# Kernel optimization log

Hardware: AMD Instinct MI355X
Metric: run time of the kernel (lower is better)

Reference implementation:

```python
import jax, jax.numpy as jnp
import numpy as np

B, T, C = 4, 2048, 1024
WIN = 16


def setup_inputs() -> dict:
    key = jax.random.key(0)
    ks = jax.random.split(key, 5)
    s = 1.0 / np.sqrt(C)
    return {
        "x": jax.random.normal(ks[0], (B, T, C), dtype=jnp.float32),
        "Wq": jax.random.normal(ks[1], (C, C), dtype=jnp.float32) * s,
        "bq": jnp.zeros((C,), jnp.float32),
        "Wk": jax.random.normal(ks[2], (C, C), dtype=jnp.float32) * s,
        "bk": jnp.zeros((C,), jnp.float32),
        "Wv": jax.random.normal(ks[3], (C, C), dtype=jnp.float32) * s,
        "bv": jnp.zeros((C,), jnp.float32),
        "Wo": jax.random.normal(ks[4], (C, C), dtype=jnp.float32) * s,
        "bo": jnp.zeros((C,), jnp.float32),
        "window": WIN,
    }


def reference(x, Wq, bq, Wk, bk, Wv, bv, Wo, bo, window):
    Bn, Tn, Cn = x.shape
    half = window // 2
    W = 2 * half + 1  # keys per query (window [t-half, t+half])
    q = x @ Wq.T + bq
    k = x @ Wk.T + bk
    v = x @ Wv.T + bv
    offs = jnp.arange(-half, half + 1)              # [W]
    tpos = jnp.arange(Tn)                            # [T]
    idx = tpos[:, None] + offs[None, :]              # [T, W]
    valid = (idx >= 0) & (idx < Tn)                  # [T, W]
    idx_c = jnp.clip(idx, 0, Tn - 1)
    k_win = k[:, idx_c, :]                           # [B, T, W, C]
    v_win = v[:, idx_c, :]                           # [B, T, W, C]
    scale = 1.0 / jnp.sqrt(jnp.asarray(Cn, x.dtype))
    scores = jnp.einsum('btc,btwc->btw', q, k_win) * scale
    scores = jnp.where(valid[None, :, :], scores, jnp.finfo(x.dtype).min)
    attn = jax.nn.softmax(scores, axis=-1)           # [B, T, W]
    ctx = jnp.einsum('btw,btwc->btc', attn, v_win)   # [B, T, C]
    return ctx @ Wo.T + bo
```

## Files before the change

### kernel.cpp

```cpp
#include <hip/hip_runtime.h>
#include <cstdint>
#include <cstddef>

#define B_ 4
#define T_ 2048
#define C_ 1024
#define M_ (B_ * T_)
#define HALF_ 8
#define W_ 17
#define QKV_STRIDE 3072

typedef unsigned short u16;
typedef _Float16 half8 __attribute__((ext_vector_type(8)));
typedef _Float16 half2_t __attribute__((ext_vector_type(2)));
typedef float f32x16 __attribute__((ext_vector_type(16)));

__device__ __forceinline__ void gload_lds16(const u16* g, u16* l) {
#if __has_builtin(__builtin_amdgcn_global_load_lds)
    __builtin_amdgcn_global_load_lds(
        (const __attribute__((address_space(1))) void*)g,
        (__attribute__((address_space(3))) void*)l, 16, 0, 0);
#else
    *(uint4*)(l + (threadIdx.x & 63) * 8) = *(const uint4*)g;
#endif
}

__device__ __forceinline__ float dot16(half8 a, half8 b, float acc) {
#if __has_builtin(__builtin_amdgcn_fdot2)
    const half2_t* pa = (const half2_t*)&a;
    const half2_t* pb = (const half2_t*)&b;
#pragma unroll
    for (int e = 0; e < 4; ++e) acc = __builtin_amdgcn_fdot2(pa[e], pb[e], acc, false);
#else
#pragma unroll
    for (int e = 0; e < 8; ++e) acc += (float)a[e] * (float)b[e];
#endif
    return acc;
}

__global__ void prologue(const float* __restrict__ x,
                         const float* __restrict__ Wq, const float* __restrict__ Wk,
                         const float* __restrict__ Wv, const float* __restrict__ Wo,
                         const float* __restrict__ bq, const float* __restrict__ bk,
                         const float* __restrict__ bv,
                         u16* __restrict__ xh, u16* __restrict__ wcat,
                         u16* __restrict__ woh, float* __restrict__ bcat) {
    const int blk = blockIdx.x;
    if (blk >= 12288) {
        int i = (blk - 12288) * 256 + threadIdx.x;
        const float* src = (i < 1024) ? bq : (i < 2048) ? bk : bv;
        bcat[i] = src[i & 1023];
        return;
    }
    const float* src;
    u16* dst;
    int j;
    if (blk < 8192)       { src = x;  dst = xh;   j = blk * 256 + threadIdx.x; }
    else if (blk < 11264) {
        int bb = blk - 8192;
        int sel = bb >> 10;
        src = (sel == 0) ? Wq : (sel == 1) ? Wk : Wv;
        dst = wcat + ((size_t)sel << 20);
        j = (bb - (sel << 10)) * 256 + threadIdx.x;
    } else                { src = Wo; dst = woh;  j = (blk - 11264) * 256 + threadIdx.x; }
    float4 v = ((const float4*)src)[j];
    ushort4 o;
    _Float16 a = (_Float16)v.x; o.x = __builtin_bit_cast(unsigned short, a);
    _Float16 b = (_Float16)v.y; o.y = __builtin_bit_cast(unsigned short, b);
    _Float16 c = (_Float16)v.z; o.z = __builtin_bit_cast(unsigned short, c);
    _Float16 d = (_Float16)v.w; o.w = __builtin_bit_cast(unsigned short, d);
    ((ushort4*)dst)[j] = o;
}

__global__ __launch_bounds__(256) void gemm_nt_lds(
    const u16* __restrict__ A, const u16* __restrict__ Bw,
    const float* __restrict__ bias, u16* __restrict__ Cout,
    int Ndim, int Kdim)
{
    __shared__ __align__(16) u16 As[128 * 32];
    __shared__ __align__(16) u16 Bs[128 * 32];

    const int tid  = threadIdx.x;
    const int lane = tid & 63;
    const int wave = tid >> 6;
    const int m0 = blockIdx.y * 128;
    const int n0 = blockIdx.x * 128;
    const int wm = (wave >> 1) * 64;
    const int wn = (wave & 1) * 64;

    const int srow = wave * 32 + (lane >> 2);
    const int kc = ((lane & 3) ^ ((lane >> 3) & 3)) * 8;
    const u16* Ap = A  + (size_t)(m0 + srow) * Kdim + kc;
    const u16* Bp = Bw + (size_t)(n0 + srow) * Kdim + kc;
    const size_t skip16 = (size_t)16 * Kdim;
    u16* AsW = As + wave * 1024;
    u16* BsW = Bs + wave * 1024;

    f32x16 acc[2][2];
#pragma unroll
    for (int i = 0; i < 2; ++i)
#pragma unroll
        for (int j = 0; j < 2; ++j)
#pragma unroll
            for (int r = 0; r < 16; ++r) acc[i][j][r] = 0.f;

    const int rr = lane & 31;
    const int hi = lane >> 5;
    const int sw = (lane >> 1) & 3;

    for (int k0 = 0; k0 < Kdim; k0 += 32) {
        __syncthreads();
        gload_lds16(Ap + k0,          AsW);
        gload_lds16(Ap + k0 + skip16, AsW + 512);
        gload_lds16(Bp + k0,          BsW);
        gload_lds16(Bp + k0 + skip16, BsW + 512);
        __syncthreads();

#pragma unroll
        for (int kk = 0; kk < 2; ++kk) {
            const int slot = ((kk * 2 + hi) ^ sw) * 8;
            half8 af[2], bf[2];
#pragma unroll
            for (int i = 0; i < 2; ++i)
                af[i] = *(const half8*)&As[(wm + i * 32 + rr) * 32 + slot];
#pragma unroll
            for (int j = 0; j < 2; ++j)
                bf[j] = *(const half8*)&Bs[(wn + j * 32 + rr) * 32 + slot];
#pragma unroll
            for (int i = 0; i < 2; ++i)
#pragma unroll
                for (int j = 0; j < 2; ++j)
                    acc[i][j] = __builtin_amdgcn_mfma_f32_32x32x16_f16(af[i], bf[j], acc[i][j], 0, 0, 0);
        }
    }

#pragma unroll
    for (int i = 0; i < 2; ++i) {
#pragma unroll
        for (int j = 0; j < 2; ++j) {
            const int col = n0 + wn + j * 32 + (lane & 31);
            const float bv = bias[col];
#pragma unroll
            for (int reg = 0; reg < 16; ++reg) {
                const int row = m0 + wm + i * 32 + (reg & 3) + 8 * (reg >> 2) + 4 * (lane >> 5);
                _Float16 h = (_Float16)(acc[i][j][reg] + bv);
                Cout[(size_t)row * Ndim + col] = __builtin_bit_cast(unsigned short, h);
            }
        }
    }
}

__global__ __launch_bounds__(256) void gemm_nt_64(
    const u16* __restrict__ A, const u16* __restrict__ Bw,
    const float* __restrict__ bias, float* __restrict__ Cout,
    int Ndim, int Kdim)
{
    __shared__ __align__(16) u16 As[128 * 32];
    __shared__ __align__(16) u16 Bs[64 * 32];

    const int tid  = threadIdx.x;
    const int lane = tid & 63;
    const int wave = tid >> 6;
    const int m0 = blockIdx.y * 128;
    const int n0 = blockIdx.x * 64;
    const int wm = (wave >> 1) * 64;
    const int wn = (wave & 1) * 32;

    const int sArow = wave * 32 + (lane >> 2);
    const int sBrow = wave * 16 + (lane >> 2);
    const int kc = ((lane & 3) ^ ((lane >> 3) & 3)) * 8;
    const u16* Ap = A  + (size_t)(m0 + sArow) * Kdim + kc;
    const u16* Bp = Bw + (size_t)(n0 + sBrow) * Kdim + kc;
    const size_t skip16 = (size_t)16 * Kdim;
    u16* AsW = As + wave * 1024;
    u16* BsW = Bs + wave * 512;

    f32x16 acc[2];
#pragma unroll
    for (int i = 0; i < 2; ++i)
#pragma unroll
        for (int r = 0; r < 16; ++r) acc[i][r] = 0.f;

    const int rr = lane & 31;
    const int hi = lane >> 5;
    const int sw = (lane >> 1) & 3;

    for (int k0 = 0; k0 < Kdim; k0 += 32) {
        __syncthreads();
        gload_lds16(Ap + k0,          AsW);
        gload_lds16(Ap + k0 + skip16, AsW + 512);
        gload_lds16(Bp + k0,          BsW);
        __syncthreads();

#pragma unroll
        for (int kk = 0; kk < 2; ++kk) {
            const int slot = ((kk * 2 + hi) ^ sw) * 8;
            half8 bf = *(const half8*)&Bs[(wn + rr) * 32 + slot];
#pragma unroll
            for (int i = 0; i < 2; ++i) {
                half8 af = *(const half8*)&As[(wm + i * 32 + rr) * 32 + slot];
                acc[i] = __builtin_amdgcn_mfma_f32_32x32x16_f16(af, bf, acc[i], 0, 0, 0);
            }
        }
    }

    const int col = n0 + wn + (lane & 31);
    const float bv = bias[col];
#pragma unroll
    for (int i = 0; i < 2; ++i) {
#pragma unroll
        for (int reg = 0; reg < 16; ++reg) {
            const int row = m0 + wm + i * 32 + (reg & 3) + 8 * (reg >> 2) + 4 * (lane >> 5);
            Cout[(size_t)row * Ndim + col] = acc[i][reg] + bv;
        }
    }
}

__global__ __launch_bounds__(256) void attn_local(
    const u16* __restrict__ qkv, u16* __restrict__ ctx)
{
    const int wid  = blockIdx.x * 4 + (threadIdx.x >> 6);
    const int lane = threadIdx.x & 63;
    const int b = wid >> 11;
    const int t = wid & (T_ - 1);
    const int base = b * T_;
    const size_t qrow = (size_t)(base + t) * QKV_STRIDE;
    const int c0 = lane * 8;

    half8 q0 = *(const half8*)(qkv + qrow + c0);
    half8 q1 = *(const half8*)(qkv + qrow + 512 + c0);

    float s[W_];
#pragma unroll
    for (int o = 0; o < W_; ++o) {
        int j = t - HALF_ + o;
        int jc = min(max(j, 0), T_ - 1);
        const size_t kb = (size_t)(base + jc) * QKV_STRIDE + 1024;
        half8 k0v = *(const half8*)(qkv + kb + c0);
        half8 k1v = *(const half8*)(qkv + kb + 512 + c0);
        float d = dot16(q1, k1v, dot16(q0, k0v, 0.f));
#pragma unroll
        for (int off = 32; off > 0; off >>= 1)
            d += __shfl_xor(d, off);
        s[o] = (j == jc) ? d * 0.03125f : -3.0e38f;
    }

    float mx = s[0];
#pragma unroll
    for (int o = 1; o < W_; ++o) mx = fmaxf(mx, s[o]);
    float den = 0.f;
#pragma unroll
    for (int o = 0; o < W_; ++o) den += __expf(s[o] - mx);
    const float inv = 1.f / den;

    float acc0[8], acc1[8];
#pragma unroll
    for (int e = 0; e < 8; ++e) { acc0[e] = 0.f; acc1[e] = 0.f; }
#pragma unroll
    for (int o = 0; o < W_; ++o) {
        int j = t - HALF_ + o;
        int jc = min(max(j, 0), T_ - 1);
        const float wt = __expf(s[o] - mx) * inv;
        const size_t vb_ = (size_t)(base + jc) * QKV_STRIDE + 2048;
        half8 v0 = *(const half8*)(qkv + vb_ + c0);
        half8 v1 = *(const half8*)(qkv + vb_ + 512 + c0);
#pragma unroll
        for (int e = 0; e < 8; ++e) {
            acc0[e] += wt * (float)v0[e];
            acc1[e] += wt * (float)v1[e];
        }
    }

    const size_t crow = (size_t)(base + t) * C_;
    half8 o0, o1;
#pragma unroll
    for (int e = 0; e < 8; ++e) { o0[e] = (_Float16)acc0[e]; o1[e] = (_Float16)acc1[e]; }
    *(half8*)(ctx + crow + c0) = o0;
    *(half8*)(ctx + crow + 512 + c0) = o1;
}

extern "C" void kernel_launch(void* const* d_in, const int* in_sizes, int n_in,
                              void* d_out, int out_size, void* d_ws, size_t ws_size,
                              hipStream_t stream) {
    const float* x  = (const float*)d_in[0];
    const float* Wq = (const float*)d_in[1];
    const float* bq = (const float*)d_in[2];
    const float* Wk = (const float*)d_in[3];
    const float* bk = (const float*)d_in[4];
    const float* Wv = (const float*)d_in[5];
    const float* bv = (const float*)d_in[6];
    const float* Wo = (const float*)d_in[7];
    const float* bo = (const float*)d_in[8];
    float* out = (float*)d_out;

    u16* xh   = (u16*)d_ws;
    u16* wcat = xh   + (size_t)M_ * C_;
    u16* woh  = wcat + (size_t)3 * C_ * C_;
    u16* qkvh = woh  + (size_t)C_ * C_;
    u16* ctxh = qkvh + (size_t)M_ * QKV_STRIDE;
    float* bcat = (float*)(ctxh + (size_t)M_ * C_);

    prologue<<<12300, 256, 0, stream>>>(x, Wq, Wk, Wv, Wo, bq, bk, bv,
                                        xh, wcat, woh, bcat);

    dim3 gqkv(QKV_STRIDE / 128, M_ / 128);
    gemm_nt_lds<<<gqkv, 256, 0, stream>>>(xh, wcat, bcat, qkvh, QKV_STRIDE, C_);

    attn_local<<<M_ / 4, 256, 0, stream>>>(qkvh, ctxh);

    dim3 go(C_ / 64, M_ / 128);
    gemm_nt_64<<<go, 256, 0, stream>>>(ctxh, woh, bo, out, C_, C_);
}
```

Measured before the change: 235.9 us.

## Register-prefetch next K tile in both GEMMs to overlap loads with MFMA

Replaces the direct global-to-LDS loads in both GEMM kernels with a register-staged software pipeline. The next K-slice is loaded into registers while MFMAs run on the current tile in LDS, so global latency is meant to be hidden behind compute instead of sitting between the two barriers. The cost is extra VGPRs for the prefetch buffers and explicit LDS writes in place of the async global_load_lds path. LDS is still single-buffered, so two barriers per iteration remain.

```diff
diff --git a/kernel.cpp b/kernel.cpp
--- a/kernel.cpp
+++ b/kernel.cpp
@@ -14,16 +14,6 @@
 typedef _Float16 half8 __attribute__((ext_vector_type(8)));
 typedef _Float16 half2_t __attribute__((ext_vector_type(2)));
 typedef float f32x16 __attribute__((ext_vector_type(16)));
-
-__device__ __forceinline__ void gload_lds16(const u16* g, u16* l) {
-#if __has_builtin(__builtin_amdgcn_global_load_lds)
-    __builtin_amdgcn_global_load_lds(
-        (const __attribute__((address_space(1))) void*)g,
-        (__attribute__((address_space(3))) void*)l, 16, 0, 0);
-#else
-    *(uint4*)(l + (threadIdx.x & 63) * 8) = *(const uint4*)g;
-#endif
-}
 
 __device__ __forceinline__ float dot16(half8 a, half8 b, float acc) {
 #if __has_builtin(__builtin_amdgcn_fdot2)
@@ -72,7 +62,7 @@
     ((ushort4*)dst)[j] = o;
 }
 
-__global__ __launch_bounds__(256) void gemm_nt_lds(
+__global__ __launch_bounds__(256) void gemm_nt_pipe(
     const u16* __restrict__ A, const u16* __restrict__ Bw,
     const float* __restrict__ bias, u16* __restrict__ Cout,
     int Ndim, int Kdim)
@@ -93,8 +83,8 @@
     const u16* Ap = A  + (size_t)(m0 + srow) * Kdim + kc;
     const u16* Bp = Bw + (size_t)(n0 + srow) * Kdim + kc;
     const size_t skip16 = (size_t)16 * Kdim;
-    u16* AsW = As + wave * 1024;
-    u16* BsW = Bs + wave * 1024;
+    u16* AsL = As + wave * 1024 + lane * 8;
+    u16* BsL = Bs + wave * 1024 + lane * 8;
 
     f32x16 acc[2][2];
 #pragma unroll
@@ -108,13 +98,25 @@
     const int hi = lane >> 5;
     const int sw = (lane >> 1) & 3;
 
+    uint4 pa0 = *(const uint4*)(Ap);
+    uint4 pa1 = *(const uint4*)(Ap + skip16);
+    uint4 pb0 = *(const uint4*)(Bp);
+    uint4 pb1 = *(const uint4*)(Bp + skip16);
+
     for (int k0 = 0; k0 < Kdim; k0 += 32) {
+        if (k0) __syncthreads();
+        *(uint4*)(AsL)       = pa0;
+        *(uint4*)(AsL + 512) = pa1;
+        *(uint4*)(BsL)       = pb0;
+        *(uint4*)(BsL + 512) = pb1;
         __syncthreads();
-        gload_lds16(Ap + k0,          AsW);
-        gload_lds16(Ap + k0 + skip16, AsW + 512);
-        gload_lds16(Bp + k0,          BsW);
-        gload_lds16(Bp + k0 + skip16, BsW + 512);
-        __syncthreads();
+
+        if (k0 + 32 < Kdim) {
+            pa0 = *(const uint4*)(Ap + k0 + 32);
+            pa1 = *(const uint4*)(Ap + k0 + 32 + skip16);
+            pb0 = *(const uint4*)(Bp + k0 + 32);
+            pb1 = *(const uint4*)(Bp + k0 + 32 + skip16);
+        }
 
 #pragma unroll
         for (int kk = 0; kk < 2; ++kk) {
@@ -150,7 +152,7 @@
     }
 }
 
-__global__ __launch_bounds__(256) void gemm_nt_64(
+__global__ __launch_bounds__(256) void gemm_nt_64_pipe(
     const u16* __restrict__ A, const u16* __restrict__ Bw,
     const float* __restrict__ bias, float* __restrict__ Cout,
     int Ndim, int Kdim)
@@ -172,8 +174,8 @@
     const u16* Ap = A  + (size_t)(m0 + sArow) * Kdim + kc;
     const u16* Bp = Bw + (size_t)(n0 + sBrow) * Kdim + kc;
     const size_t skip16 = (size_t)16 * Kdim;
-    u16* AsW = As + wave * 1024;
-    u16* BsW = Bs + wave * 512;
+    u16* AsL = As + wave * 1024 + lane * 8;
+    u16* BsL = Bs + wave * 512  + lane * 8;
 
     f32x16 acc[2];
 #pragma unroll
@@ -185,12 +187,22 @@
     const int hi = lane >> 5;
     const int sw = (lane >> 1) & 3;
 
+    uint4 pa0 = *(const uint4*)(Ap);
+    uint4 pa1 = *(const uint4*)(Ap + skip16);
+    uint4 pb0 = *(const uint4*)(Bp);
+
     for (int k0 = 0; k0 < Kdim; k0 += 32) {
+        if (k0) __syncthreads();
+        *(uint4*)(AsL)       = pa0;
+        *(uint4*)(AsL + 512) = pa1;
+        *(uint4*)(BsL)       = pb0;
         __syncthreads();
-        gload_lds16(Ap + k0,          AsW);
-        gload_lds16(Ap + k0 + skip16, AsW + 512);
-        gload_lds16(Bp + k0,          BsW);
-        __syncthreads();
+
+        if (k0 + 32 < Kdim) {
+            pa0 = *(const uint4*)(Ap + k0 + 32);
+            pa1 = *(const uint4*)(Ap + k0 + 32 + skip16);
+            pb0 = *(const uint4*)(Bp + k0 + 32);
+        }
 
 #pragma unroll
         for (int kk = 0; kk < 2; ++kk) {
@@ -304,10 +316,10 @@
                                         xh, wcat, woh, bcat);
 
     dim3 gqkv(QKV_STRIDE / 128, M_ / 128);
-    gemm_nt_lds<<<gqkv, 256, 0, stream>>>(xh, wcat, bcat, qkvh, QKV_STRIDE, C_);
+    gemm_nt_pipe<<<gqkv, 256, 0, stream>>>(xh, wcat, bcat, qkvh, QKV_STRIDE, C_);
 
     attn_local<<<M_ / 4, 256, 0, stream>>>(qkvh, ctxh);
 
     dim3 go(C_ / 64, M_ / 128);
-    gemm_nt_64<<<go, 256, 0, stream>>>(ctxh, woh, bo, out, C_, C_);
-}
+    gemm_nt_64_pipe<<<go, 256, 0, stream>>>(ctxh, woh, bo, out, C_, C_);
+}
```

Result: no change. 238.7 us (+1.2%).
